# Performance work log

Measured on AMD Instinct MI355X. Metric: run time of the kernel, lower is better.

The kernel has to match this reference:

```python
import jax, jax.numpy as jnp
import numpy as np
import math

# BDH config (defaults from BDHConfig)
D = 256        # n_embd
NH = 4         # n_head
MULT = 128     # mlp_internal_dim_multiplier
N = MULT * D // NH   # 8192 latent dim per head
NLAYER = 6
VOCAB = 256
B, T = 1, 1024
THETA = 2.0 ** 16
TWO_PI = 2.0 * math.pi


def _freqs(n):
    # get_freqs: quantize exponent to even integers
    t = jnp.arange(n, dtype=jnp.float32)
    q = jnp.floor(t / 2.0) * 2.0
    return 1.0 / (THETA ** (q / n)) / TWO_PI  # [N]


def _ln(x, eps=1e-5):
    # LayerNorm without affine params (elementwise_affine=False)
    m = jnp.mean(x, axis=-1, keepdims=True)
    v = jnp.mean((x - m) ** 2, axis=-1, keepdims=True)
    return (x - m) / jnp.sqrt(v + eps)


def _rope(phases, v):
    # phases: [T,N] broadcastable to v [...,T,N]
    ph = (phases % 1.0) * TWO_PI
    cos, sin = jnp.cos(ph), jnp.sin(ph)
    # rotate adjacent pairs: (-v_odd, v_even) interleaved
    vrot = jnp.stack((-v[..., 1::2], v[..., ::2]), axis=-1).reshape(v.shape)
    return v * cos + vrot * sin


def setup_inputs() -> dict:
    key = jax.random.key(0)
    ks = jax.random.split(key, 6)
    std = 0.02
    return {
        "idx": jax.random.randint(ks[0], (B, T), 0, VOCAB),
        "embed_w": jax.random.normal(ks[1], (VOCAB, D), jnp.float32) * std,
        "encoder": jax.random.normal(ks[2], (NH, D, N), jnp.float32) * std,
        "encoder_v": jax.random.normal(ks[3], (NH, D, N), jnp.float32) * std,
        "decoder": jax.random.normal(ks[4], (NH * N, D), jnp.float32) * std,
        "lm_head": jax.random.normal(ks[5], (D, VOCAB), jnp.float32) * std,
    }


def reference(idx, embed_w, encoder, encoder_v, decoder, lm_head):
    freqs = _freqs(N)                                             # [N]
    phases = jnp.arange(T, dtype=jnp.float32)[:, None] * freqs    # [T,N]
    mask = jnp.tril(jnp.ones((T, T), jnp.float32), k=-1)          # strict causal
    dec = decoder.reshape(NH, N, D)

    x = _ln(embed_w[idx])                                         # [B,T,D]
    for _ in range(NLAYER):
        x_sp = jax.nn.relu(jnp.einsum('btd,hdn->bhtn', x, encoder))   # [B,nh,T,N]
        qr = _rope(phases, x_sp)                                       # [B,nh,T,N]
        scores = jnp.einsum('bhtn,bhsn->bhts', qr, qr) * mask          # [B,nh,T,T]
        ykv = _ln(jnp.einsum('bhts,bsd->bhtd', scores, x))             # [B,nh,T,D]
        y_sp = jax.nn.relu(jnp.einsum('bhtd,hdn->bhtn', ykv, encoder_v))
        xy = x_sp * y_sp                                               # [B,nh,T,N]
        ymlp = jnp.einsum('bhtn,hnd->btd', xy, dec)                    # [B,T,D]
        x = _ln(x + _ln(ymlp))
    return x @ lm_head                                                 # [B,T,VOCAB]
```

## Files before the change

kernel.cpp:

```cpp
#include <hip/hip_runtime.h>
#include <hip/hip_bf16.h>
#include <math.h>

#define T_ 1024
#define D_ 256
#define N_ 8192
#define NH_ 4
#define NLAYER_ 6
#define VOCAB_ 256
#define TWO_PI_F 6.283185307179586f

typedef __attribute__((ext_vector_type(8))) short short8;
typedef __attribute__((ext_vector_type(4))) float floatx4;
typedef unsigned short ushort_t;

__device__ __forceinline__ void cp16(const void* g, void* l) {
    __builtin_amdgcn_global_load_lds((const __attribute__((address_space(1))) unsigned int*)g,
                                     (__attribute__((address_space(3))) unsigned int*)l,
                                     16, 0, 0);
}

__device__ __forceinline__ float bf2f_raw(unsigned short u) {
    union { unsigned int i; float f; } x;
    x.i = ((unsigned int)u) << 16;
    return x.f;
}
__device__ __forceinline__ unsigned int f2bf_u(float f) {
    union { float f; unsigned int u; } x; x.f = f;
    return (x.u + 0x7fffu + ((x.u >> 16) & 1u)) >> 16;
}

__device__ __forceinline__ float block_sum(float v, float* red) {
    int tid = threadIdx.x;
    red[tid] = v;
    __syncthreads();
    #pragma unroll
    for (int s = 128; s > 0; s >>= 1) {
        if (tid < s) red[tid] += red[tid + s];
        __syncthreads();
    }
    float r = red[0];
    __syncthreads();
    return r;
}


__global__ void k_embed_ln(const int* __restrict__ idx, const float* __restrict__ ew,
                           float* __restrict__ x, __hip_bfloat16* __restrict__ x_bf) {
    __shared__ float red[256];
    int t = blockIdx.x, d = threadIdx.x;
    float v = ew[idx[t] * D_ + d];
    float mean = block_sum(v, red) * (1.0f / D_);
    float c = v - mean;
    float var = block_sum(c * c, red) * (1.0f / D_);
    float o = c * rsqrtf(var + 1e-5f);
    x[t * D_ + d] = o;
    x_bf[t * D_ + d] = __float2bfloat16(o);
}

__global__ void k_ln_rows(const float* __restrict__ yp, __hip_bfloat16* __restrict__ outb) {
    __shared__ float red[256];
    int r = blockIdx.x, d = threadIdx.x;
    const size_t S = (size_t)NH_ * T_ * D_;
    float v = yp[(size_t)r * D_ + d] + yp[S + (size_t)r * D_ + d];
    float mean = block_sum(v, red) * (1.0f / D_);
    float c = v - mean;
    float var = block_sum(c * c, red) * (1.0f / D_);
    outb[(size_t)r * D_ + d] = __float2bfloat16(c * rsqrtf(var + 1e-5f));
}

__global__ void k_x_update(float* __restrict__ x, const float* __restrict__ ypart,
                           __hip_bfloat16* __restrict__ x_bf) {
    __shared__ float red[256];
    int t = blockIdx.x, d = threadIdx.x;
    float v = 0.0f;
    #pragma unroll
    for (int i = 0; i < 32; i++) v += ypart[(size_t)i * T_ * D_ + t * D_ + d];
    float m1 = block_sum(v, red) * (1.0f / D_);
    float c1 = v - m1;
    float v1 = block_sum(c1 * c1, red) * (1.0f / D_);
    float u = c1 * rsqrtf(v1 + 1e-5f);
    float w = x[t * D_ + d] + u;
    float m2 = block_sum(w, red) * (1.0f / D_);
    float c2 = w - m2;
    float v2 = block_sum(c2 * c2, red) * (1.0f / D_);
    float o = c2 * rsqrtf(v2 + 1e-5f);
    x[t * D_ + d] = o;
    x_bf[t * D_ + d] = __float2bfloat16(o);
}

__global__ __launch_bounds__(256) void k_tcvt(const float* __restrict__ in,
                                              __hip_bfloat16* __restrict__ out,
                                              int R, int C) {
    int h = blockIdx.z;
    int r0 = blockIdx.y * 32, c0 = blockIdx.x * 32;
    __shared__ float tile[32][33];
    int tx = threadIdx.x & 31, ty = threadIdx.x >> 5;
    const float* inh = in + (size_t)h * R * C;
    __hip_bfloat16* outh = out + (size_t)h * R * C;
    #pragma unroll
    for (int i = 0; i < 4; i++)
        tile[ty + 8 * i][tx] = inh[(size_t)(r0 + ty + 8 * i) * C + c0 + tx];
    __syncthreads();
    #pragma unroll
    for (int i = 0; i < 4; i++)
        outh[(size_t)(c0 + ty + 8 * i) * R + r0 + tx] = __float2bfloat16(tile[tx][ty + 8 * i]);
}

__global__ void k_rope_tab(unsigned int* __restrict__ tab) {
    int idx = blockIdx.x * 256 + threadIdx.x;
    int t = idx >> 12, j = idx & 4095;
    float freq = exp2f((float)j * (-1.0f / 256.0f)) * 0.15915494309189535f;
    float ph = (float)t * freq;
    ph -= floorf(ph);
    float s, c;
    __sincosf(ph * TWO_PI_F, &s, &c);
    tab[idx] = f2bf_u(c) | (f2bf_u(s) << 16);
}

__device__ __forceinline__ void gemm128(const ushort_t* __restrict__ A,
                                        const ushort_t* __restrict__ B,
                                        int lda, int ldb, int K,
                                        ushort_t* As, ushort_t* Bs,
                                        floatx4 acc[4][4]) {
    const int tid = threadIdx.x;
    const int lane = tid & 63, wid = tid >> 6;
    const int wm = wid >> 1, wn = wid & 1;
    const int quad = lane >> 4, col = lane & 15;
    int srow[4], scol[4];
    #pragma unroll
    for (int i = 0; i < 4; i++) {
        int s = i * 256 + tid;
        srow[i] = s >> 3;
        scol[i] = (s & 7) ^ (srow[i] & 7);
    }
    for (int k0 = 0; k0 < K; k0 += 64) {
        #pragma unroll
        for (int i = 0; i < 4; i++)
            cp16(A + (size_t)srow[i] * lda + k0 + scol[i] * 8,
                 As + (size_t)(i * 256 + wid * 64) * 8);
        #pragma unroll
        for (int i = 0; i < 4; i++)
            cp16(B + (size_t)srow[i] * ldb + k0 + scol[i] * 8,
                 Bs + (size_t)(i * 256 + wid * 64) * 8);
        __syncthreads();
        #pragma unroll
        for (int kk = 0; kk < 2; kk++) {
            short8 af[4], bf[4];
            #pragma unroll
            for (int mi = 0; mi < 4; mi++) {
                int row = wm * 64 + mi * 16 + col;
                int pc = ((kk << 2) + quad) ^ (row & 7);
                af[mi] = *(const short8*)&As[row * 64 + pc * 8];
            }
            #pragma unroll
            for (int ni = 0; ni < 4; ni++) {
                int row = wn * 64 + ni * 16 + col;
                int pc = ((kk << 2) + quad) ^ (row & 7);
                bf[ni] = *(const short8*)&Bs[row * 64 + pc * 8];
            }
            #pragma unroll
            for (int mi = 0; mi < 4; mi++)
                #pragma unroll
                for (int ni = 0; ni < 4; ni++)
                    acc[mi][ni] = __builtin_amdgcn_mfma_f32_16x16x32_bf16(
                        af[mi], bf[ni], acc[mi][ni], 0, 0, 0);
        }
        __syncthreads();
    }
}

#define GEMM_PROLOGUE()                                              \
    __shared__ __align__(16) ushort_t As[128 * 64];                  \
    __shared__ __align__(16) ushort_t Bs[128 * 64];                  \
    floatx4 acc[4][4];                                               \
    _Pragma("unroll") for (int mi = 0; mi < 4; mi++)                 \
        _Pragma("unroll") for (int ni = 0; ni < 4; ni++)             \
            acc[mi][ni] = (floatx4){0.f, 0.f, 0.f, 0.f};             \
    const int lane = threadIdx.x & 63, wid = threadIdx.x >> 6;       \
    const int wm = wid >> 1, wn = wid & 1;                           \
    const int quad = lane >> 4, col = lane & 15;                     \
    const int odd = lane & 1;                                        \
    const int rsel = odd ? 2 : 0, rother = odd ? 0 : 2;

__global__ __launch_bounds__(256) void k_scores_m(const __hip_bfloat16* __restrict__ qr,
                                                  __hip_bfloat16* __restrict__ scp) {
    const int b = blockIdx.x;
    const int ks = b & 3, h = (b >> 2) & 3;
    int i = b >> 4;
    int ti = 0;
    while ((ti + 1) * (ti + 2) / 2 <= i) ti++;
    int si = i - ti * (ti + 1) / 2;
    const int t0 = ti * 128, s0 = si * 128;
    GEMM_PROLOGUE();
    const ushort_t* qh = (const ushort_t*)qr + (size_t)h * T_ * N_ + (size_t)ks * (N_ / 4);
    gemm128(qh + (size_t)t0 * N_, qh + (size_t)s0 * N_, N_, N_, N_ / 4, As, Bs, acc);
    unsigned int* sch = (unsigned int*)(scp + (size_t)ks * NH_ * T_ * T_ + (size_t)h * T_ * T_);
    #pragma unroll
    for (int mi = 0; mi < 4; mi++)
        #pragma unroll
        for (int ni = 0; ni < 4; ni++) {
            const int ss = s0 + wn * 64 + ni * 16 + col;
            const int ss_e = ss & ~1;
            const int rowb = t0 + wm * 64 + mi * 16 + quad * 4;
            #pragma unroll
            for (int rr = 0; rr < 2; rr++) {
                int tt_o = rowb + rother + rr;
                float send = (ss < tt_o) ? acc[mi][ni][rother + rr] : 0.0f;
                float recv = __shfl_xor(send, 1);
                int tt = rowb + rsel + rr;
                float mine = (ss < tt) ? acc[mi][ni][rsel + rr] : 0.0f;
                float lo = odd ? recv : mine, hi = odd ? mine : recv;
                sch[((size_t)tt * T_ + ss_e) >> 1] = f2bf_u(lo) | (f2bf_u(hi) << 16);
            }
        }
}

__global__ void k_sc_cvt(__hip_bfloat16* __restrict__ scp) {
    int i = blockIdx.x;
    int ti = 0;
    while ((ti + 1) * (ti + 2) / 2 <= i) ti++;
    int si = i - ti * (ti + 1) / 2;
    const size_t S2h = (size_t)NH_ * T_ * T_ / 2;
    unsigned int* sp = (unsigned int*)scp;
    size_t b = (size_t)blockIdx.y * T_ * T_ / 2;
    for (int e = threadIdx.x; e < 128 * 64; e += 256) {
        int r = e >> 6, c = e & 63;
        size_t off = b + (((size_t)(ti * 128 + r) * T_ + si * 128) >> 1) + c;
        float lo = 0.f, hi = 0.f;
        #pragma unroll
        for (int s = 0; s < 4; s++) {
            unsigned int w = sp[off + s * S2h];
            lo += bf2f_raw((unsigned short)(w & 0xffff));
            hi += bf2f_raw((unsigned short)(w >> 16));
        }
        sp[off] = f2bf_u(lo) | (f2bf_u(hi) << 16);
    }
}

template <int MODE>
__global__ __launch_bounds__(256) void k_proj_m(const __hip_bfloat16* __restrict__ Abf,
                                                const __hip_bfloat16* __restrict__ Wt,
                                                __hip_bfloat16* __restrict__ out1,
                                                __hip_bfloat16* __restrict__ out2,
                                                const __hip_bfloat16* __restrict__ xsp,
                                                const unsigned int* __restrict__ rtab) {
    const int h = blockIdx.z;
    const int t0 = blockIdx.y * 128, n0 = blockIdx.x * 128;
    GEMM_PROLOGUE();
    const ushort_t* Ah = (const ushort_t*)Abf + (MODE ? (size_t)h * T_ * D_ : (size_t)0)
                         + (size_t)t0 * D_;
    const ushort_t* Bh = (const ushort_t*)Wt + (size_t)h * N_ * D_ + (size_t)n0 * D_;
    gemm128(Ah, Bh, D_, D_, D_, As, Bs, acc);
    unsigned int* o1 = (unsigned int*)out1;
    unsigned int* o2 = (unsigned int*)out2;
    #pragma unroll
    for (int mi = 0; mi < 4; mi++)
        #pragma unroll
        for (int ni = 0; ni < 4; ni++) {
            const int nn_e = (n0 + wn * 64 + ni * 16 + col) & ~1;
            const int rowb = t0 + wm * 64 + mi * 16 + quad * 4;
            #pragma unroll
            for (int rr = 0; rr < 2; rr++) {
                float send = fmaxf(acc[mi][ni][rother + rr], 0.0f);
                float recv = __shfl_xor(send, 1);
                float mine = fmaxf(acc[mi][ni][rsel + rr], 0.0f);
                float ve = odd ? recv : mine, vo = odd ? mine : recv;
                int tt = rowb + rsel + rr;
                size_t o32 = (((size_t)h * T_ + tt) * (size_t)N_ + nn_e) >> 1;
                if (MODE == 0) {
                    o1[o32] = f2bf_u(ve) | (f2bf_u(vo) << 16);
                    unsigned int cs = rtab[(size_t)tt * 4096 + (nn_e >> 1)];
                    float c = bf2f_raw((unsigned short)(cs & 0xffff));
                    float s = bf2f_raw((unsigned short)(cs >> 16));
                    o2[o32] = f2bf_u(ve * c - vo * s) | (f2bf_u(vo * c + ve * s) << 16);
                } else {
                    unsigned int xw = ((const unsigned int*)xsp)[o32];
                    float xe = bf2f_raw((unsigned short)(xw & 0xffff));
                    float xo = bf2f_raw((unsigned short)(xw >> 16));
                    o1[o32] = f2bf_u(ve * xe) | (f2bf_u(vo * xo) << 16);
                }
            }
        }
}

__global__ __launch_bounds__(256) void k_ykv_m(const __hip_bfloat16* __restrict__ sc,
                                               const __hip_bfloat16* __restrict__ xT,
                                               float* __restrict__ ykvp) {
    const int b = blockIdx.x;
    const int h = (b >> 1) & 3, ks = b & 1;
    const int r0 = b >> 3;
    const int d0 = (r0 & 1) * 128, t0 = (r0 >> 1) * 128;
    GEMM_PROLOGUE();
    const int half = (t0 + 128) >> 1;
    const ushort_t* Ah = (const ushort_t*)sc + (size_t)h * T_ * T_ + (size_t)t0 * T_ + ks * half;
    const ushort_t* Bh = (const ushort_t*)xT + (size_t)d0 * T_ + ks * half;
    gemm128(Ah, Bh, T_, T_, half, As, Bs, acc);
    float2* yp = (float2*)(ykvp + (size_t)ks * NH_ * T_ * D_);
    #pragma unroll
    for (int mi = 0; mi < 4; mi++)
        #pragma unroll
        for (int ni = 0; ni < 4; ni++) {
            const int dd_e = (d0 + wn * 64 + ni * 16 + col) & ~1;
            const int rowb = t0 + wm * 64 + mi * 16 + quad * 4;
            #pragma unroll
            for (int rr = 0; rr < 2; rr++) {
                float send = acc[mi][ni][rother + rr];
                float recv = __shfl_xor(send, 1);
                float mine = acc[mi][ni][rsel + rr];
                int tt = rowb + rsel + rr;
                yp[(((size_t)h * T_ + tt) * D_ + dd_e) >> 1] =
                    odd ? make_float2(recv, mine) : make_float2(mine, recv);
            }
        }
}

__global__ __launch_bounds__(256) void k_ymlp_m(const __hip_bfloat16* __restrict__ xy,
                                                const __hip_bfloat16* __restrict__ decT,
                                                float* __restrict__ ypart) {
    const int b = blockIdx.x;
    const int slice = b & 31;
    const int ks = slice >> 2, h = slice & 3;
    const int r0 = b >> 5;
    const int d0 = (r0 & 1) * 128, t0 = (r0 >> 1) * 128;
    GEMM_PROLOGUE();
    const ushort_t* Ah = (const ushort_t*)xy + (size_t)h * T_ * N_ + (size_t)t0 * N_ + ks * 1024;
    const ushort_t* Bh = (const ushort_t*)decT + (size_t)h * D_ * N_ + (size_t)d0 * N_ + ks * 1024;
    gemm128(Ah, Bh, N_, N_, 1024, As, Bs, acc);
    float2* yp = (float2*)(ypart + (size_t)slice * T_ * D_);
    #pragma unroll
    for (int mi = 0; mi < 4; mi++)
        #pragma unroll
        for (int ni = 0; ni < 4; ni++) {
            const int dd_e = (d0 + wn * 64 + ni * 16 + col) & ~1;
            const int rowb = t0 + wm * 64 + mi * 16 + quad * 4;
            #pragma unroll
            for (int rr = 0; rr < 2; rr++) {
                float send = acc[mi][ni][rother + rr];
                float recv = __shfl_xor(send, 1);
                float mine = acc[mi][ni][rsel + rr];
                int tt = rowb + rsel + rr;
                yp[((size_t)tt * D_ + dd_e) >> 1] =
                    odd ? make_float2(recv, mine) : make_float2(mine, recv);
            }
        }
}

__global__ __launch_bounds__(256) void k_lmhead_m(const __hip_bfloat16* __restrict__ x_bf,
                                                  const __hip_bfloat16* __restrict__ lmT,
                                                  float* __restrict__ out) {
    const int v0 = blockIdx.x * 128, t0 = blockIdx.y * 128;
    GEMM_PROLOGUE();
    const ushort_t* Ah = (const ushort_t*)x_bf + (size_t)t0 * D_;
    const ushort_t* Bh = (const ushort_t*)lmT + (size_t)v0 * D_;
    gemm128(Ah, Bh, D_, D_, D_, As, Bs, acc);
    float2* op = (float2*)out;
    #pragma unroll
    for (int mi = 0; mi < 4; mi++)
        #pragma unroll
        for (int ni = 0; ni < 4; ni++) {
            const int vv_e = (v0 + wn * 64 + ni * 16 + col) & ~1;
            const int rowb = t0 + wm * 64 + mi * 16 + quad * 4;
            #pragma unroll
            for (int rr = 0; rr < 2; rr++) {
                float send = acc[mi][ni][rother + rr];
                float recv = __shfl_xor(send, 1);
                float mine = acc[mi][ni][rsel + rr];
                int tt = rowb + rsel + rr;
                op[((size_t)tt * VOCAB_ + vv_e) >> 1] =
                    odd ? make_float2(recv, mine) : make_float2(mine, recv);
            }
        }
}


extern "C" void kernel_launch(void* const* d_in, const int* in_sizes, int n_in,
                              void* d_out, int out_size, void* d_ws, size_t ws_size,
                              hipStream_t stream) {
    const int* idx = (const int*)d_in[0];
    const float* embed_w = (const float*)d_in[1];
    const float* encoder = (const float*)d_in[2];
    const float* encoder_v = (const float*)d_in[3];
    const float* decoder = (const float*)d_in[4];
    const float* lm_head = (const float*)d_in[5];
    float* out = (float*)d_out;

    char* p = (char*)d_ws;
    auto alloc = [&](size_t bytes) {
        char* q = p;
        p += (bytes + 255) & ~(size_t)255;
        return q;
    };
    float* x = (float*)alloc((size_t)T_ * D_ * 4);
    __hip_bfloat16* x_bf = (__hip_bfloat16*)alloc((size_t)T_ * D_ * 2);
    __hip_bfloat16* xT = (__hip_bfloat16*)alloc((size_t)T_ * D_ * 2);
    __hip_bfloat16* ykv_bf = (__hip_bfloat16*)alloc((size_t)NH_ * T_ * D_ * 2);
    __hip_bfloat16* scp = (__hip_bfloat16*)alloc((size_t)4 * NH_ * T_ * T_ * 2);
    __hip_bfloat16* xsp = (__hip_bfloat16*)alloc((size_t)NH_ * T_ * N_ * 2);
    __hip_bfloat16* qr = (__hip_bfloat16*)alloc((size_t)NH_ * T_ * N_ * 2);
    __hip_bfloat16* encT = (__hip_bfloat16*)alloc((size_t)NH_ * N_ * D_ * 2);
    __hip_bfloat16* encvT = (__hip_bfloat16*)alloc((size_t)NH_ * N_ * D_ * 2);
    __hip_bfloat16* decT = (__hip_bfloat16*)alloc((size_t)NH_ * N_ * D_ * 2);
    __hip_bfloat16* lmT = (__hip_bfloat16*)alloc((size_t)VOCAB_ * D_ * 2);
    unsigned int* rtab = (unsigned int*)alloc((size_t)T_ * 4096 * 4);
    float* ypart = (float*)xsp;
    float* ykvp = (float*)(scp + (size_t)NH_ * T_ * T_);

    k_tcvt<<<dim3(N_ / 32, D_ / 32, NH_), 256, 0, stream>>>(encoder, encT, D_, N_);
    k_tcvt<<<dim3(N_ / 32, D_ / 32, NH_), 256, 0, stream>>>(encoder_v, encvT, D_, N_);
    k_tcvt<<<dim3(D_ / 32, N_ / 32, NH_), 256, 0, stream>>>(decoder, decT, N_, D_);
    k_tcvt<<<dim3(VOCAB_ / 32, D_ / 32, 1), 256, 0, stream>>>(lm_head, lmT, D_, VOCAB_);
    k_rope_tab<<<T_ * 4096 / 256, 256, 0, stream>>>(rtab);

    k_embed_ln<<<T_, 256, 0, stream>>>(idx, embed_w, x, x_bf);
    for (int l = 0; l < NLAYER_; l++) {
        k_proj_m<0><<<dim3(N_ / 128, T_ / 128, NH_), 256, 0, stream>>>(x_bf, encT, xsp, qr,
                                                                       nullptr, rtab);
        k_scores_m<<<36 * 16, 256, 0, stream>>>(qr, scp);
        k_sc_cvt<<<dim3(36, NH_), 256, 0, stream>>>(scp);
        k_tcvt<<<dim3(D_ / 32, T_ / 32, 1), 256, 0, stream>>>(x, xT, T_, D_);
        k_ykv_m<<<16 * 8, 256, 0, stream>>>(scp, xT, ykvp);
        k_ln_rows<<<NH_ * T_, 256, 0, stream>>>(ykvp, ykv_bf);
        k_proj_m<1><<<dim3(N_ / 128, T_ / 128, NH_), 256, 0, stream>>>(ykv_bf, encvT, qr ,
                                                                       nullptr, xsp, rtab);
        k_ymlp_m<<<16 * 32, 256, 0, stream>>>(qr, decT, ypart);
        k_x_update<<<T_, 256, 0, stream>>>(x, ypart, x_bf);
    }
    k_lmhead_m<<<dim3(VOCAB_ / 128, T_ / 128), 256, 0, stream>>>(x_bf, lmT, out);
}
```

Before: 1.326 ms.

## Drop x_sp buffer by inverse-rotating qr; store ymlp partials in bf16

The first projection now writes only the rotated qr tensor, and the second projection recovers x_sp by applying the inverse RoPE rotation to qr read back in place. This removes one 64MB bf16 write per layer and a separate buffer. The ymlp split-K partials are stored as bf16 instead of fp32, halving that traffic. The cost is extra rope-table reads in the second projection and extra rounding error, both from reconstructing x_sp out of bf16 qr and from the bf16 partial sums.

```diff
diff --git a/kernel.cpp b/kernel.cpp
--- a/kernel.cpp
+++ b/kernel.cpp
@@ -69,13 +69,16 @@
     outb[(size_t)r * D_ + d] = __float2bfloat16(c * rsqrtf(var + 1e-5f));
 }
 
-__global__ void k_x_update(float* __restrict__ x, const float* __restrict__ ypart,
+__global__ void k_x_update(float* __restrict__ x, const unsigned int* __restrict__ ypart,
                            __hip_bfloat16* __restrict__ x_bf) {
     __shared__ float red[256];
     int t = blockIdx.x, d = threadIdx.x;
     float v = 0.0f;
     #pragma unroll
-    for (int i = 0; i < 32; i++) v += ypart[(size_t)i * T_ * D_ + t * D_ + d];
+    for (int i = 0; i < 32; i++) {
+        unsigned int w = ypart[(size_t)i * (T_ * D_ / 2) + t * (D_ / 2) + (d >> 1)];
+        v += bf2f_raw((unsigned short)((d & 1) ? (w >> 16) : (w & 0xffff)));
+    }
     float m1 = block_sum(v, red) * (1.0f / D_);
     float c1 = v - m1;
     float v1 = block_sum(c1 * c1, red) * (1.0f / D_);
@@ -242,8 +245,6 @@
 __global__ __launch_bounds__(256) void k_proj_m(const __hip_bfloat16* __restrict__ Abf,
                                                 const __hip_bfloat16* __restrict__ Wt,
                                                 __hip_bfloat16* __restrict__ out1,
-                                                __hip_bfloat16* __restrict__ out2,
-                                                const __hip_bfloat16* __restrict__ xsp,
                                                 const unsigned int* __restrict__ rtab) {
     const int h = blockIdx.z;
     const int t0 = blockIdx.y * 128, n0 = blockIdx.x * 128;
@@ -253,7 +254,6 @@
     const ushort_t* Bh = (const ushort_t*)Wt + (size_t)h * N_ * D_ + (size_t)n0 * D_;
     gemm128(Ah, Bh, D_, D_, D_, As, Bs, acc);
     unsigned int* o1 = (unsigned int*)out1;
-    unsigned int* o2 = (unsigned int*)out2;
     #pragma unroll
     for (int mi = 0; mi < 4; mi++)
         #pragma unroll
@@ -268,16 +268,17 @@
                 float ve = odd ? recv : mine, vo = odd ? mine : recv;
                 int tt = rowb + rsel + rr;
                 size_t o32 = (((size_t)h * T_ + tt) * (size_t)N_ + nn_e) >> 1;
+                unsigned int cs = rtab[(size_t)tt * 4096 + (nn_e >> 1)];
+                float c = bf2f_raw((unsigned short)(cs & 0xffff));
+                float s = bf2f_raw((unsigned short)(cs >> 16));
                 if (MODE == 0) {
-                    o1[o32] = f2bf_u(ve) | (f2bf_u(vo) << 16);
-                    unsigned int cs = rtab[(size_t)tt * 4096 + (nn_e >> 1)];
-                    float c = bf2f_raw((unsigned short)(cs & 0xffff));
-                    float s = bf2f_raw((unsigned short)(cs >> 16));
-                    o2[o32] = f2bf_u(ve * c - vo * s) | (f2bf_u(vo * c + ve * s) << 16);
+                    o1[o32] = f2bf_u(ve * c - vo * s) | (f2bf_u(vo * c + ve * s) << 16);
                 } else {
-                    unsigned int xw = ((const unsigned int*)xsp)[o32];
-                    float xe = bf2f_raw((unsigned short)(xw & 0xffff));
-                    float xo = bf2f_raw((unsigned short)(xw >> 16));
+                    unsigned int qw = o1[o32];
+                    float qe = bf2f_raw((unsigned short)(qw & 0xffff));
+                    float qo = bf2f_raw((unsigned short)(qw >> 16));
+                    float xe = qe * c + qo * s;
+                    float xo = qo * c - qe * s;
                     o1[o32] = f2bf_u(ve * xe) | (f2bf_u(vo * xo) << 16);
                 }
             }
@@ -317,7 +318,7 @@
 
 __global__ __launch_bounds__(256) void k_ymlp_m(const __hip_bfloat16* __restrict__ xy,
                                                 const __hip_bfloat16* __restrict__ decT,
-                                                float* __restrict__ ypart) {
+                                                unsigned int* __restrict__ ypart) {
     const int b = blockIdx.x;
     const int slice = b & 31;
     const int ks = slice >> 2, h = slice & 3;
@@ -327,7 +328,7 @@
     const ushort_t* Ah = (const ushort_t*)xy + (size_t)h * T_ * N_ + (size_t)t0 * N_ + ks * 1024;
     const ushort_t* Bh = (const ushort_t*)decT + (size_t)h * D_ * N_ + (size_t)d0 * N_ + ks * 1024;
     gemm128(Ah, Bh, N_, N_, 1024, As, Bs, acc);
-    float2* yp = (float2*)(ypart + (size_t)slice * T_ * D_);
+    unsigned int* yp = ypart + (size_t)slice * (T_ * D_ / 2);
     #pragma unroll
     for (int mi = 0; mi < 4; mi++)
         #pragma unroll
@@ -339,9 +340,9 @@
                 float send = acc[mi][ni][rother + rr];
                 float recv = __shfl_xor(send, 1);
                 float mine = acc[mi][ni][rsel + rr];
+                float lo = odd ? recv : mine, hi = odd ? mine : recv;
                 int tt = rowb + rsel + rr;
-                yp[((size_t)tt * D_ + dd_e) >> 1] =
-                    odd ? make_float2(recv, mine) : make_float2(mine, recv);
+                yp[((size_t)tt * D_ + dd_e) >> 1] = f2bf_u(lo) | (f2bf_u(hi) << 16);
             }
         }
 }
@@ -396,14 +397,13 @@
     __hip_bfloat16* xT = (__hip_bfloat16*)alloc((size_t)T_ * D_ * 2);
     __hip_bfloat16* ykv_bf = (__hip_bfloat16*)alloc((size_t)NH_ * T_ * D_ * 2);
     __hip_bfloat16* scp = (__hip_bfloat16*)alloc((size_t)4 * NH_ * T_ * T_ * 2);
-    __hip_bfloat16* xsp = (__hip_bfloat16*)alloc((size_t)NH_ * T_ * N_ * 2);
     __hip_bfloat16* qr = (__hip_bfloat16*)alloc((size_t)NH_ * T_ * N_ * 2);
+    unsigned int* ypart = (unsigned int*)alloc((size_t)32 * T_ * D_ * 2);
     __hip_bfloat16* encT = (__hip_bfloat16*)alloc((size_t)NH_ * N_ * D_ * 2);
     __hip_bfloat16* encvT = (__hip_bfloat16*)alloc((size_t)NH_ * N_ * D_ * 2);
     __hip_bfloat16* decT = (__hip_bfloat16*)alloc((size_t)NH_ * N_ * D_ * 2);
     __hip_bfloat16* lmT = (__hip_bfloat16*)alloc((size_t)VOCAB_ * D_ * 2);
     unsigned int* rtab = (unsigned int*)alloc((size_t)T_ * 4096 * 4);
-    float* ypart = (float*)xsp;
     float* ykvp = (float*)(scp + (size_t)NH_ * T_ * T_);
 
     k_tcvt<<<dim3(N_ / 32, D_ / 32, NH_), 256, 0, stream>>>(encoder, encT, D_, N_);
@@ -414,15 +414,13 @@
 
     k_embed_ln<<<T_, 256, 0, stream>>>(idx, embed_w, x, x_bf);
     for (int l = 0; l < NLAYER_; l++) {
-        k_proj_m<0><<<dim3(N_ / 128, T_ / 128, NH_), 256, 0, stream>>>(x_bf, encT, xsp, qr,
-                                                                       nullptr, rtab);
+        k_proj_m<0><<<dim3(N_ / 128, T_ / 128, NH_), 256, 0, stream>>>(x_bf, encT, qr, rtab);
         k_scores_m<<<36 * 16, 256, 0, stream>>>(qr, scp);
         k_sc_cvt<<<dim3(36, NH_), 256, 0, stream>>>(scp);
         k_tcvt<<<dim3(D_ / 32, T_ / 32, 1), 256, 0, stream>>>(x, xT, T_, D_);
         k_ykv_m<<<16 * 8, 256, 0, stream>>>(scp, xT, ykvp);
         k_ln_rows<<<NH_ * T_, 256, 0, stream>>>(ykvp, ykv_bf);
-        k_proj_m<1><<<dim3(N_ / 128, T_ / 128, NH_), 256, 0, stream>>>(ykv_bf, encvT, qr ,
-                                                                       nullptr, xsp, rtab);
+        k_proj_m<1><<<dim3(N_ / 128, T_ / 128, NH_), 256, 0, stream>>>(ykv_bf, encvT, qr, rtab);
         k_ymlp_m<<<16 * 32, 256, 0, stream>>>(qr, decT, ypart);
         k_x_update<<<T_, 256, 0, stream>>>(x, ypart, x_bf);
     }
```

Result: slower. 1.465 ms (+10.5%).
